# Kernel optimization log

Hardware: AMD Instinct MI355X
Metric: run time of the kernel (lower is better)

The kernel has to match this reference:

```python
import jax, jax.numpy as jnp
import numpy as np

SR = 44100.0  # sample_rate from init_kwargs


def _alpha(tau_ms):
    # Eq. (10): alpha = exp(-1 / (tau_s * fs)), tau clamped to [0.1, 1000] ms
    tau_s = jnp.clip(tau_ms, 0.1, 1000.0) / 1000.0
    return jnp.exp(-1.0 / (tau_s * SR))


def _env(x, alpha, attack):
    # Nonlinear envelope follower (Eqs. 9-10).
    # attack=True  -> smooth attack (when |x| rising), instant decay
    # attack=False -> smooth decay  (when |x| falling), instant attack
    xa = jnp.abs(x)
    xs = jnp.moveaxis(xa, -1, 0)  # [T, B, C]
    y0 = jnp.zeros(xa.shape[:-1], xa.dtype)  # [B, C]

    def step(y_prev, xn):
        cond = (xn > y_prev) if attack else (xn < y_prev)
        y_curr = jnp.where(cond, (1.0 - alpha) * xn + alpha * y_prev, xn)
        return y_curr, y_curr

    _, ys = jax.lax.scan(step, y0, xs)
    return jnp.moveaxis(ys, 0, -1)  # [B, C, T]


def _db_to_amp(db):
    return jnp.power(10.0, db / 20.0)


def reference(x, tauAtc, tauDtc, nu, dBregDelta):
    # Temporal Contrast Enhancement (Weger et al., ICAD 2019, Eqs. 12-14).
    # high_pass_filter is the identity in the source, so sh = x.
    alpha_d = _alpha(jnp.clip(tauDtc, 1.0, 100.0))
    alpha_a = _alpha(jnp.clip(tauAtc, 1.0, 100.0))
    et_d = _env(x, alpha_d, attack=False)      # envd(sh)
    et_a = _env(et_d, alpha_a, attack=True)    # enva(et_d)
    nu_amp = _db_to_amp(jnp.clip(nu, -60.0, 0.0))
    et = jnp.maximum(et_d - et_a - nu_amp, 0.0)
    et_env = _env(et, alpha_d, attack=False)   # envd(et)
    reg = _db_to_amp(jnp.clip(dBregDelta, -120.0, -60.0))
    modulation = et / (et_env + reg)
    return x * modulation


def setup_inputs() -> dict:
    key = jax.random.key(0)
    x = jax.random.normal(key, (8, 32, 88200), dtype=jnp.float32)  # [B, C, T]
    return {
        "x": x,
        "tauAtc": jnp.float32(3.0),
        "tauDtc": jnp.float32(7.0),
        "nu": jnp.float32(-40.0),
        "dBregDelta": jnp.float32(-96.0),
    }
```

## Files before the change

### kernel.cpp

```cpp
#include <hip/hip_runtime.h>
#include <cmath>


typedef float f32x4 __attribute__((ext_vector_type(4)));

static constexpr int   kT  = 88200;
static constexpr float kSR = 44100.0f;

static constexpr int FS_      = 24;
static constexpr int FNC_     = kT / FS_;
static constexpr int FPADS    = FS_ + 4;
static constexpr int FTH      = 512;
static constexpr int FNT      = (FNC_ + FTH - 1) / FTH;
static constexpr int FTAILC   = FNC_ - FTH * (FNT - 1);
static constexpr int FF4C     = FS_ / 4;
static constexpr int FTILE_F4 = FTH * FF4C;
static constexpr int FTAIL_F4 = FTAILC * FF4C;
static constexpr int FBUF_F   = FTH * FPADS;

struct EnvP { float ad, bd, aa, ba, nuamp, reg; };

__device__ __forceinline__ EnvP make_params(const float* tauA, const float* tauD,
                                            const float* nu, const float* dbreg) {
  EnvP p;
  float td = fminf(fmaxf(tauD[0], 1.0f), 100.0f);
  td = fminf(fmaxf(td, 0.1f), 1000.0f) * 0.001f;
  float ta = fminf(fmaxf(tauA[0], 1.0f), 100.0f);
  ta = fminf(fmaxf(ta, 0.1f), 1000.0f) * 0.001f;
  p.ad = expf(-1.0f / (td * kSR));
  p.aa = expf(-1.0f / (ta * kSR));
  p.bd = 1.0f - p.ad;
  p.ba = 1.0f - p.aa;
  p.nuamp = exp10f(fminf(fmaxf(nu[0],    -60.0f),   0.0f) * 0.05f);
  p.reg   = exp10f(fminf(fmaxf(dbreg[0], -120.0f), -60.0f) * 0.05f);
  return p;
}

template <int MODE>
__device__ __forceinline__ void sweep(const float* __restrict__ xs,
                                      float* __restrict__ os,
                                      const EnvP& p,
                                      float* __restrict__ buf0,
                                      float* __restrict__ buf1,
                                      float* __restrict__ Ac, float* __restrict__ Bc,
                                      const float* __restrict__ Ydl,
                                      const float* __restrict__ Yal,
                                      const float* __restrict__ Yel,
                                      int t) {
  f32x4 r0, r1, r2, r3, r4, r5;
  const f32x4* xg4 = reinterpret_cast<const f32x4*>(xs);

#define LD_TILE(TILE)                                                        \
  do {                                                                       \
    const int nf4_ = ((TILE) == FNT - 1) ? FTAIL_F4 : FTILE_F4;              \
    const f32x4* xg_ = xg4 + (size_t)(TILE) * FTILE_F4;                      \
    int i0_ = t;                                                             \
    r0 = xg_[i0_ < nf4_ ? i0_ : 0];  i0_ += FTH;                             \
    r1 = xg_[i0_ < nf4_ ? i0_ : 0];  i0_ += FTH;                             \
    r2 = xg_[i0_ < nf4_ ? i0_ : 0];  i0_ += FTH;                             \
    r3 = xg_[i0_ < nf4_ ? i0_ : 0];  i0_ += FTH;                             \
    r4 = xg_[i0_ < nf4_ ? i0_ : 0];  i0_ += FTH;                             \
    r5 = xg_[i0_ < nf4_ ? i0_ : 0];                                          \
  } while (0)

#define WR_TILE(BUF)                                                         \
  do {                                                                       \
    float* b_ = (BUF);                                                       \
    int i0_ = t, ch_, of_;                                                   \
    ch_ = i0_ / FF4C; of_ = (i0_ - ch_ * FF4C) * 4;                          \
    *reinterpret_cast<f32x4*>(&b_[ch_ * FPADS + of_]) = r0;  i0_ += FTH;     \
    ch_ = i0_ / FF4C; of_ = (i0_ - ch_ * FF4C) * 4;                          \
    *reinterpret_cast<f32x4*>(&b_[ch_ * FPADS + of_]) = r1;  i0_ += FTH;     \
    ch_ = i0_ / FF4C; of_ = (i0_ - ch_ * FF4C) * 4;                          \
    *reinterpret_cast<f32x4*>(&b_[ch_ * FPADS + of_]) = r2;  i0_ += FTH;     \
    ch_ = i0_ / FF4C; of_ = (i0_ - ch_ * FF4C) * 4;                          \
    *reinterpret_cast<f32x4*>(&b_[ch_ * FPADS + of_]) = r3;  i0_ += FTH;     \
    ch_ = i0_ / FF4C; of_ = (i0_ - ch_ * FF4C) * 4;                          \
    *reinterpret_cast<f32x4*>(&b_[ch_ * FPADS + of_]) = r4;  i0_ += FTH;     \
    ch_ = i0_ / FF4C; of_ = (i0_ - ch_ * FF4C) * 4;                          \
    *reinterpret_cast<f32x4*>(&b_[ch_ * FPADS + of_]) = r5;                  \
  } while (0)

  LD_TILE(0);
  WR_TILE(buf0);
  __syncthreads();
  int cur = 0;
  for (int it = 0; it < FNT; ++it) {
    const bool pf = (it + 1 < FNT);
    if (pf) LD_TILE(it + 1);
    __builtin_amdgcn_sched_barrier(0);
    float* bc = cur ? buf1 : buf0;
    float* bn = cur ? buf0 : buf1;
    const int c = it * FTH + t;
    if (c < FNC_) {
      float* my = &bc[t * FPADS];
      if (MODE == 0) {
        float A = -INFINITY, B = 0.0f;
#pragma unroll 2
        for (int i = 0; i < FF4C; ++i) {
          f32x4 v = *reinterpret_cast<const f32x4*>(&my[4 * i]);
#pragma unroll
          for (int j = 0; j < 4; ++j) {
            float xa = fabsf(v[j]);
            float bx = p.bd * xa;
            A = fmaxf(xa, fmaf(p.ad, A, bx));
            B = fmaf(p.ad, B, bx);
          }
        }
        Ac[c] = A; Bc[c] = B;
      } else if (MODE == 1) {
        float yd = Ydl[c];
        float A = INFINITY, B = 0.0f;
#pragma unroll 2
        for (int i = 0; i < FF4C; ++i) {
          f32x4 v = *reinterpret_cast<const f32x4*>(&my[4 * i]);
#pragma unroll
          for (int j = 0; j < 4; ++j) {
            float xa = fabsf(v[j]);
            yd = fmaxf(xa, fmaf(p.ad, yd, p.bd * xa));
            float by = p.ba * yd;
            A = fminf(yd, fmaf(p.aa, A, by));
            B = fmaf(p.aa, B, by);
          }
        }
        Ac[c] = A; Bc[c] = B;
      } else if (MODE == 2) {
        float yd = Ydl[c], ya = Yal[c];
        float A = -INFINITY, B = 0.0f;
#pragma unroll 2
        for (int i = 0; i < FF4C; ++i) {
          f32x4 v = *reinterpret_cast<const f32x4*>(&my[4 * i]);
#pragma unroll
          for (int j = 0; j < 4; ++j) {
            float xa = fabsf(v[j]);
            yd = fmaxf(xa, fmaf(p.ad, yd, p.bd * xa));
            ya = fminf(yd, fmaf(p.aa, ya, p.ba * yd));
            float et = fmaxf((yd - ya) - p.nuamp, 0.0f);
            float bx = p.bd * et;
            A = fmaxf(et, fmaf(p.ad, A, bx));
            B = fmaf(p.ad, B, bx);
          }
        }
        Ac[c] = A; Bc[c] = B;
      } else {
        float yd = Ydl[c], ya = Yal[c], ye = Yel[c];
#pragma unroll 2
        for (int i = 0; i < FF4C; ++i) {
          f32x4 v = *reinterpret_cast<const f32x4*>(&my[4 * i]);
          f32x4 oo;
#pragma unroll
          for (int j = 0; j < 4; ++j) {
            float xa = fabsf(v[j]);
            yd = fmaxf(xa, fmaf(p.ad, yd, p.bd * xa));
            ya = fminf(yd, fmaf(p.aa, ya, p.ba * yd));
            float et = fmaxf((yd - ya) - p.nuamp, 0.0f);
            ye = fmaxf(et, fmaf(p.ad, ye, p.bd * et));
            oo[j] = v[j] * (et / (ye + p.reg));
          }
          *reinterpret_cast<f32x4*>(&my[4 * i]) = oo;
        }
      }
    }
    if (MODE == 3) {
      __syncthreads();
      f32x4* og = reinterpret_cast<f32x4*>(os) + (size_t)it * FTILE_F4;
      const int nf4 = pf ? FTILE_F4 : FTAIL_F4;
#pragma unroll
      for (int i = 0; i < FF4C; ++i) {
        int idx = t + i * FTH;
        if (idx < nf4) {
          int chunk = idx / FF4C;
          int off   = (idx - chunk * FF4C) * 4;
          f32x4 v = *reinterpret_cast<const f32x4*>(&bc[chunk * FPADS + off]);
          __builtin_nontemporal_store(v, &og[idx]);
        }
      }
    }
    if (pf) WR_TILE(bn);
    __syncthreads();
    cur ^= 1;
  }
#undef LD_TILE
#undef WR_TILE
}

template <int ATTACK>
__device__ __forceinline__ void scan_lds(const float* __restrict__ Ac,
                                         const float* __restrict__ Bc,
                                         float* __restrict__ Y,
                                         const EnvP& p,
                                         float* __restrict__ sbuf, int t) {
  constexpr int CPT = (FNC_ + FTH - 1) / FTH;
  const float alpha = ATTACK ? p.aa : p.ad;
  const float ID_A  = ATTACK ? INFINITY : -INFINITY;
  const float gS = powf(alpha, (float)FS_);

  float ca[CPT], cb[CPT];
  float a = ID_A, b = 0.0f, g = 1.0f;
#pragma unroll
  for (int k = 0; k < CPT; ++k) {
    int c = t * CPT + k;
    if (c < FNC_) { ca[k] = Ac[c]; cb[k] = Bc[c]; }
    else          { ca[k] = ID_A;  cb[k] = 0.0f; }
    float cg = (c < FNC_) ? gS : 1.0f;
    float na = ATTACK ? fminf(ca[k], fmaf(cg, a, cb[k]))
                      : fmaxf(ca[k], fmaf(cg, a, cb[k]));
    b = fmaf(cg, b, cb[k]);
    g = cg * g;
    a = na;
  }

  float* sA = sbuf; float* sB = sbuf + FTH; float* sG = sbuf + 2 * FTH;
  sA[t] = a; sB[t] = b; sG[t] = g;
  __syncthreads();
#pragma unroll
  for (int d = 1; d < FTH; d <<= 1) {
    float pa = 0.0f, pb = 0.0f, pg = 0.0f;
    if (t >= d) { pa = sA[t - d]; pb = sB[t - d]; pg = sG[t - d]; }
    __syncthreads();
    if (t >= d) {
      float na = ATTACK ? fminf(a, fmaf(g, pa, b)) : fmaxf(a, fmaf(g, pa, b));
      b = fmaf(g, pb, b);
      g = g * pg;
      a = na;
      sA[t] = a; sB[t] = b; sG[t] = g;
    }
    __syncthreads();
  }

  float ea, eb;
  if (t == 0) { ea = ID_A; eb = 0.0f; }
  else        { ea = sA[t - 1]; eb = sB[t - 1]; }

#pragma unroll
  for (int k = 0; k < CPT; ++k) {
    int c = t * CPT + k;
    if (c >= FNC_) break;
    Y[c] = ATTACK ? fminf(ea, eb) : fmaxf(ea, eb);
    float na = ATTACK ? fminf(ca[k], fmaf(gS, ea, cb[k]))
                      : fmaxf(ca[k], fmaf(gS, ea, cb[k]));
    eb = fmaf(gS, eb, cb[k]);
    ea = na;
  }
}

__global__
__attribute__((amdgpu_flat_work_group_size(512, 512), amdgpu_waves_per_eu(2, 2)))
void k_one(const float* __restrict__ x,
           const float* tauA, const float* tauD,
           const float* nu, const float* dbreg,
           float* __restrict__ Ydg, float* __restrict__ Yag,
           float* __restrict__ Yeg,
           float* __restrict__ out) {
  extern __shared__ float lds[];
  float* buf0 = lds;
  float* buf1 = lds + FBUF_F;
  float* Ac   = lds + 2 * FBUF_F;
  float* Bc   = Ac + FNC_;
  const int t = threadIdx.x;
  const int s = blockIdx.x;
  const float* xs = x   + (size_t)s * kT;
  float*       os = out + (size_t)s * kT;
  float* Yd = Ydg + (size_t)s * FNC_;
  float* Ya = Yag + (size_t)s * FNC_;
  float* Ye = Yeg + (size_t)s * FNC_;
  EnvP p = make_params(tauA, tauD, nu, dbreg);

  sweep<0>(xs, nullptr, p, buf0, buf1, Ac, Bc, nullptr, nullptr, nullptr, t);
  scan_lds<0>(Ac, Bc, Yd, p, buf0, t);
  __syncthreads();
  sweep<1>(xs, nullptr, p, buf0, buf1, Ac, Bc, Yd, nullptr, nullptr, t);
  scan_lds<1>(Ac, Bc, Ya, p, buf0, t);
  __syncthreads();
  sweep<2>(xs, nullptr, p, buf0, buf1, Ac, Bc, Yd, Ya, nullptr, t);
  scan_lds<0>(Ac, Bc, Ye, p, buf0, t);
  __syncthreads();
  sweep<3>(xs, os, p, buf0, buf1, Ac, Bc, Yd, Ya, Ye, t);
}

template <int FS, int MODE>
__global__ __launch_bounds__(256)
void k_pass(const float* __restrict__ x,
            const float* tauA, const float* tauD,
            const float* nu, const float* dbreg,
            const float* __restrict__ FYd, const float* __restrict__ FYa,
            const float* __restrict__ FYe,
            float* __restrict__ O0, float* __restrict__ O1) {
  constexpr int FP = FS + 4;
  __shared__ float lds[256 * FP];
  const int t   = threadIdx.x;
  const int blk = blockIdx.x;
  const size_t tileBase = (size_t)blk * (256 * FS);
  const float4* xg = reinterpret_cast<const float4*>(x + tileBase);
#pragma unroll
  for (int i = 0; i < FS / 4; ++i) {
    int idx = t + i * 256;
    float4 v = xg[idx];
    int chunk = (idx * 4) / FS;
    int off   = idx * 4 - chunk * FS;
    *reinterpret_cast<float4*>(&lds[chunk * FP + off]) = v;
  }
  __syncthreads();
  EnvP p = make_params(tauA, tauD, nu, dbreg);
  const int gchunk = blk * 256 + t;
  float* my = &lds[t * FP];
  if (MODE == 0) {
    float A = -INFINITY, B = 0.0f;
#pragma unroll 2
    for (int i = 0; i < FS / 4; ++i) {
      float4 v = *reinterpret_cast<const float4*>(&my[4 * i]);
      float vv[4] = {v.x, v.y, v.z, v.w};
#pragma unroll
      for (int j = 0; j < 4; ++j) {
        float xa = fabsf(vv[j]);
        float bx = p.bd * xa;
        A = fmaxf(xa, fmaf(p.ad, A, bx));
        B = fmaf(p.ad, B, bx);
      }
    }
    O0[gchunk] = A; O1[gchunk] = B;
  } else if (MODE == 1) {
    float yd = FYd[gchunk];
    float A = INFINITY, B = 0.0f;
#pragma unroll 2
    for (int i = 0; i < FS / 4; ++i) {
      float4 v = *reinterpret_cast<const float4*>(&my[4 * i]);
      float vv[4] = {v.x, v.y, v.z, v.w};
#pragma unroll
      for (int j = 0; j < 4; ++j) {
        float xa = fabsf(vv[j]);
        yd = fmaxf(xa, fmaf(p.ad, yd, p.bd * xa));
        float by = p.ba * yd;
        A = fminf(yd, fmaf(p.aa, A, by));
        B = fmaf(p.aa, B, by);
      }
    }
    O0[gchunk] = A; O1[gchunk] = B;
  } else if (MODE == 2) {
    float yd = FYd[gchunk], ya = FYa[gchunk];
    float A = -INFINITY, B = 0.0f;
#pragma unroll 2
    for (int i = 0; i < FS / 4; ++i) {
      float4 v = *reinterpret_cast<const float4*>(&my[4 * i]);
      float vv[4] = {v.x, v.y, v.z, v.w};
#pragma unroll
      for (int j = 0; j < 4; ++j) {
        float xa = fabsf(vv[j]);
        yd = fmaxf(xa, fmaf(p.ad, yd, p.bd * xa));
        ya = fminf(yd, fmaf(p.aa, ya, p.ba * yd));
        float et = fmaxf((yd - ya) - p.nuamp, 0.0f);
        float bx = p.bd * et;
        A = fmaxf(et, fmaf(p.ad, A, bx));
        B = fmaf(p.ad, B, bx);
      }
    }
    O0[gchunk] = A; O1[gchunk] = B;
  } else {
    float yd = FYd[gchunk], ya = FYa[gchunk], ye = FYe[gchunk];
#pragma unroll 2
    for (int i = 0; i < FS / 4; ++i) {
      float4 v = *reinterpret_cast<const float4*>(&my[4 * i]);
      float vv[4] = {v.x, v.y, v.z, v.w};
      float oo[4];
#pragma unroll
      for (int j = 0; j < 4; ++j) {
        float xa = fabsf(vv[j]);
        yd = fmaxf(xa, fmaf(p.ad, yd, p.bd * xa));
        ya = fminf(yd, fmaf(p.aa, ya, p.ba * yd));
        float et = fmaxf((yd - ya) - p.nuamp, 0.0f);
        ye = fmaxf(et, fmaf(p.ad, ye, p.bd * et));
        oo[j] = vv[j] * (et / (ye + p.reg));
      }
      *reinterpret_cast<float4*>(&my[4 * i]) = make_float4(oo[0], oo[1], oo[2], oo[3]);
    }
    __syncthreads();
    float4* og = reinterpret_cast<float4*>(O0 + tileBase);
#pragma unroll
    for (int i = 0; i < FS / 4; ++i) {
      int idx = t + i * 256;
      int chunk = (idx * 4) / FS;
      int off   = idx * 4 - chunk * FS;
      og[idx] = *reinterpret_cast<const float4*>(&lds[chunk * FP + off]);
    }
  }
}

template <int FS, int ATTACK>
__global__ __launch_bounds__(256)
void k_scan(const float* __restrict__ A, const float* __restrict__ B,
            float* __restrict__ Y,
            const float* tauA, const float* tauD,
            const float* nu, const float* dbreg) {
  constexpr int FNC = kT / FS;
  constexpr int CPT = (FNC + 255) / 256;
  EnvP p = make_params(tauA, tauD, nu, dbreg);
  const float alpha = ATTACK ? p.aa : p.ad;
  const float ID_A  = ATTACK ? INFINITY : -INFINITY;
  int s = blockIdx.x, t = threadIdx.x;
  long base = (long)s * FNC;
  float gS = powf(alpha, (float)FS);

  float ca[CPT], cb[CPT];
  float a = ID_A, b = 0.0f, g = 1.0f;
#pragma unroll
  for (int k = 0; k < CPT; ++k) {
    int c = t * CPT + k;
    if (c < FNC) { ca[k] = A[base + c]; cb[k] = B[base + c]; }
    else         { ca[k] = ID_A;        cb[k] = 0.0f; }
    float cg = (c < FNC) ? gS : 1.0f;
    float na = ATTACK ? fminf(ca[k], fmaf(cg, a, cb[k]))
                      : fmaxf(ca[k], fmaf(cg, a, cb[k]));
    b = fmaf(cg, b, cb[k]);
    g = cg * g;
    a = na;
  }

  __shared__ float sA[256], sB[256], sG[256];
  sA[t] = a; sB[t] = b; sG[t] = g;
  __syncthreads();
#pragma unroll
  for (int d = 1; d < 256; d <<= 1) {
    float pa = 0.0f, pb = 0.0f, pg = 0.0f;
    if (t >= d) { pa = sA[t - d]; pb = sB[t - d]; pg = sG[t - d]; }
    __syncthreads();
    if (t >= d) {
      float na = ATTACK ? fminf(a, fmaf(g, pa, b)) : fmaxf(a, fmaf(g, pa, b));
      b = fmaf(g, pb, b);
      g = g * pg;
      a = na;
      sA[t] = a; sB[t] = b; sG[t] = g;
    }
    __syncthreads();
  }

  float ea, eb;
  if (t == 0) { ea = ID_A; eb = 0.0f; }
  else        { ea = sA[t - 1]; eb = sB[t - 1]; }

#pragma unroll
  for (int k = 0; k < CPT; ++k) {
    int c = t * CPT + k;
    if (c >= FNC) break;
    Y[base + c] = ATTACK ? fminf(ea, eb) : fmaxf(ea, eb);
    float na = ATTACK ? fminf(ca[k], fmaf(gS, ea, cb[k]))
                      : fmaxf(ca[k], fmaf(gS, ea, cb[k]));
    eb = fmaf(gS, eb, cb[k]);
    ea = na;
  }
}

template <int FS>
static void run_pipeline(const float* x, const float* tauA, const float* tauD,
                         const float* nu, const float* dbreg, float* out,
                         float* wsf, int nseries, hipStream_t stream) {
  const int nc  = kT / FS;
  const int nch = nseries * nc;
  float* A   = wsf;
  float* B   = wsf + (size_t)nch;
  float* FYd = wsf + (size_t)2 * nch;
  float* FYa = wsf + (size_t)3 * nch;
  float* FYe = wsf + (size_t)4 * nch;
  const int grid = nch / 256;

  k_pass<FS, 0><<<grid, 256, 0, stream>>>(x, tauA, tauD, nu, dbreg, nullptr, nullptr, nullptr, A, B);
  k_scan<FS, 0><<<nseries, 256, 0, stream>>>(A, B, FYd, tauA, tauD, nu, dbreg);
  k_pass<FS, 1><<<grid, 256, 0, stream>>>(x, tauA, tauD, nu, dbreg, FYd, nullptr, nullptr, A, B);
  k_scan<FS, 1><<<nseries, 256, 0, stream>>>(A, B, FYa, tauA, tauD, nu, dbreg);
  k_pass<FS, 2><<<grid, 256, 0, stream>>>(x, tauA, tauD, nu, dbreg, FYd, FYa, nullptr, A, B);
  k_scan<FS, 0><<<nseries, 256, 0, stream>>>(A, B, FYe, tauA, tauD, nu, dbreg);
  k_pass<FS, 3><<<grid, 256, 0, stream>>>(x, tauA, tauD, nu, dbreg, FYd, FYa, FYe, out, nullptr);
}

extern "C" void kernel_launch(void* const* d_in, const int* in_sizes, int n_in,
                              void* d_out, int out_size, void* d_ws, size_t ws_size,
                              hipStream_t stream) {
  const float* x     = (const float*)d_in[0];
  const float* tauA  = (const float*)d_in[1];
  const float* tauD  = (const float*)d_in[2];
  const float* nu    = (const float*)d_in[3];
  const float* dbreg = (const float*)d_in[4];
  float* out = (float*)d_out;
  float* wsf = (float*)d_ws;
  const int nseries = in_sizes[0] / kT;

  constexpr size_t LDSZ = (size_t)(2 * FBUF_F + 2 * FNC_) * sizeof(float);
  const size_t NS = (size_t)FNC_ * nseries;
  const bool wsOK = 3 * NS * sizeof(float) <= ws_size;

  static int fusedOK = -1;
  if (fusedOK < 0) {
    hipFuncSetAttribute(reinterpret_cast<const void*>(&k_one),
                        hipFuncAttributeMaxDynamicSharedMemorySize, (int)LDSZ);
    (void)hipGetLastError();
    fusedOK = 1;
  }

  if (fusedOK == 1 && wsOK) {
    float* Yd = wsf;
    float* Ya = wsf + NS;
    float* Ye = wsf + 2 * NS;
    k_one<<<nseries, FTH, LDSZ, stream>>>(x, tauA, tauD, nu, dbreg, Yd, Ya, Ye, out);
    if (hipGetLastError() == hipSuccess) return;
    fusedOK = 0;
  }

  auto fits = [&](int FS) {
    return (size_t)5 * nseries * (kT / FS) * sizeof(float) <= ws_size;
  };
  if      (fits(40))  run_pipeline<40 >(x, tauA, tauD, nu, dbreg, out, wsf, nseries, stream);
  else if (fits(56))  run_pipeline<56 >(x, tauA, tauD, nu, dbreg, out, wsf, nseries, stream);
  else if (fits(72))  run_pipeline<72 >(x, tauA, tauD, nu, dbreg, out, wsf, nseries, stream);
  else                run_pipeline<120>(x, tauA, tauD, nu, dbreg, out, wsf, nseries, stream);
}
```

Before: 226.8 us.

## Replace LDS double-buffered tile staging with direct per-thread global loads

The fused per-series kernel no longer stages input tiles through double-buffered LDS with a register prefetch. Each thread now loads its 24-sample chunk directly from global memory as six float4 loads, and in the final pass writes output straight to global with nontemporal stores. Block size doubles to 1024 threads with static LDS, and the dynamic-LDS attribute setup and fallback check are dropped. This removes LDS traffic and most barriers, but each thread's loads are strided across lanes, so coalescing is worse and latency hiding now depends on occupancy instead of explicit prefetch.

Result: slower. 400.2 us (+76.4%).

```diff
diff --git a/kernel.cpp b/kernel.cpp
--- a/kernel.cpp
+++ b/kernel.cpp
@@ -7,16 +7,11 @@
 static constexpr int   kT  = 88200;
 static constexpr float kSR = 44100.0f;
 
-static constexpr int FS_      = 24;
-static constexpr int FNC_     = kT / FS_;
-static constexpr int FPADS    = FS_ + 4;
-static constexpr int FTH      = 512;
-static constexpr int FNT      = (FNC_ + FTH - 1) / FTH;
-static constexpr int FTAILC   = FNC_ - FTH * (FNT - 1);
-static constexpr int FF4C     = FS_ / 4;
-static constexpr int FTILE_F4 = FTH * FF4C;
-static constexpr int FTAIL_F4 = FTAILC * FF4C;
-static constexpr int FBUF_F   = FTH * FPADS;
+static constexpr int FS_    = 24;
+static constexpr int FNC_   = kT / FS_;
+static constexpr int FTH    = 1024;
+static constexpr int FNT    = (FNC_ + FTH - 1) / FTH;
+static constexpr int FF4C   = FS_ / 4;
 
 struct EnvP { float ad, bd, aa, ba, nuamp, reg; };
 
@@ -40,148 +35,87 @@
 __device__ __forceinline__ void sweep(const float* __restrict__ xs,
                                       float* __restrict__ os,
                                       const EnvP& p,
-                                      float* __restrict__ buf0,
-                                      float* __restrict__ buf1,
                                       float* __restrict__ Ac, float* __restrict__ Bc,
                                       const float* __restrict__ Ydl,
                                       const float* __restrict__ Yal,
                                       const float* __restrict__ Yel,
                                       int t) {
-  f32x4 r0, r1, r2, r3, r4, r5;
   const f32x4* xg4 = reinterpret_cast<const f32x4*>(xs);
-
-#define LD_TILE(TILE)                                                        \
-  do {                                                                       \
-    const int nf4_ = ((TILE) == FNT - 1) ? FTAIL_F4 : FTILE_F4;              \
-    const f32x4* xg_ = xg4 + (size_t)(TILE) * FTILE_F4;                      \
-    int i0_ = t;                                                             \
-    r0 = xg_[i0_ < nf4_ ? i0_ : 0];  i0_ += FTH;                             \
-    r1 = xg_[i0_ < nf4_ ? i0_ : 0];  i0_ += FTH;                             \
-    r2 = xg_[i0_ < nf4_ ? i0_ : 0];  i0_ += FTH;                             \
-    r3 = xg_[i0_ < nf4_ ? i0_ : 0];  i0_ += FTH;                             \
-    r4 = xg_[i0_ < nf4_ ? i0_ : 0];  i0_ += FTH;                             \
-    r5 = xg_[i0_ < nf4_ ? i0_ : 0];                                          \
-  } while (0)
-
-#define WR_TILE(BUF)                                                         \
-  do {                                                                       \
-    float* b_ = (BUF);                                                       \
-    int i0_ = t, ch_, of_;                                                   \
-    ch_ = i0_ / FF4C; of_ = (i0_ - ch_ * FF4C) * 4;                          \
-    *reinterpret_cast<f32x4*>(&b_[ch_ * FPADS + of_]) = r0;  i0_ += FTH;     \
-    ch_ = i0_ / FF4C; of_ = (i0_ - ch_ * FF4C) * 4;                          \
-    *reinterpret_cast<f32x4*>(&b_[ch_ * FPADS + of_]) = r1;  i0_ += FTH;     \
-    ch_ = i0_ / FF4C; of_ = (i0_ - ch_ * FF4C) * 4;                          \
-    *reinterpret_cast<f32x4*>(&b_[ch_ * FPADS + of_]) = r2;  i0_ += FTH;     \
-    ch_ = i0_ / FF4C; of_ = (i0_ - ch_ * FF4C) * 4;                          \
-    *reinterpret_cast<f32x4*>(&b_[ch_ * FPADS + of_]) = r3;  i0_ += FTH;     \
-    ch_ = i0_ / FF4C; of_ = (i0_ - ch_ * FF4C) * 4;                          \
-    *reinterpret_cast<f32x4*>(&b_[ch_ * FPADS + of_]) = r4;  i0_ += FTH;     \
-    ch_ = i0_ / FF4C; of_ = (i0_ - ch_ * FF4C) * 4;                          \
-    *reinterpret_cast<f32x4*>(&b_[ch_ * FPADS + of_]) = r5;                  \
-  } while (0)
-
-  LD_TILE(0);
-  WR_TILE(buf0);
-  __syncthreads();
-  int cur = 0;
+#pragma unroll
   for (int it = 0; it < FNT; ++it) {
-    const bool pf = (it + 1 < FNT);
-    if (pf) LD_TILE(it + 1);
-    __builtin_amdgcn_sched_barrier(0);
-    float* bc = cur ? buf1 : buf0;
-    float* bn = cur ? buf0 : buf1;
     const int c = it * FTH + t;
     if (c < FNC_) {
-      float* my = &bc[t * FPADS];
+      const f32x4* xc = xg4 + (size_t)c * FF4C;
+      f32x4 v0 = xc[0], v1 = xc[1], v2 = xc[2],
+            v3 = xc[3], v4 = xc[4], v5 = xc[5];
       if (MODE == 0) {
         float A = -INFINITY, B = 0.0f;
-#pragma unroll 2
-        for (int i = 0; i < FF4C; ++i) {
-          f32x4 v = *reinterpret_cast<const f32x4*>(&my[4 * i]);
-#pragma unroll
-          for (int j = 0; j < 4; ++j) {
-            float xa = fabsf(v[j]);
-            float bx = p.bd * xa;
-            A = fmaxf(xa, fmaf(p.ad, A, bx));
-            B = fmaf(p.ad, B, bx);
-          }
-        }
+#define STEP0(V)                                                             \
+  _Pragma("unroll")                                                          \
+  for (int j = 0; j < 4; ++j) {                                              \
+    float xa = fabsf((V)[j]);                                                \
+    float bx = p.bd * xa;                                                    \
+    A = fmaxf(xa, fmaf(p.ad, A, bx));                                        \
+    B = fmaf(p.ad, B, bx);                                                   \
+  }
+        STEP0(v0) STEP0(v1) STEP0(v2) STEP0(v3) STEP0(v4) STEP0(v5)
+#undef STEP0
         Ac[c] = A; Bc[c] = B;
       } else if (MODE == 1) {
         float yd = Ydl[c];
         float A = INFINITY, B = 0.0f;
-#pragma unroll 2
-        for (int i = 0; i < FF4C; ++i) {
-          f32x4 v = *reinterpret_cast<const f32x4*>(&my[4 * i]);
-#pragma unroll
-          for (int j = 0; j < 4; ++j) {
-            float xa = fabsf(v[j]);
-            yd = fmaxf(xa, fmaf(p.ad, yd, p.bd * xa));
-            float by = p.ba * yd;
-            A = fminf(yd, fmaf(p.aa, A, by));
-            B = fmaf(p.aa, B, by);
-          }
-        }
+#define STEP1(V)                                                             \
+  _Pragma("unroll")                                                          \
+  for (int j = 0; j < 4; ++j) {                                              \
+    float xa = fabsf((V)[j]);                                                \
+    yd = fmaxf(xa, fmaf(p.ad, yd, p.bd * xa));                               \
+    float by = p.ba * yd;                                                    \
+    A = fminf(yd, fmaf(p.aa, A, by));                                        \
+    B = fmaf(p.aa, B, by);                                                   \
+  }
+        STEP1(v0) STEP1(v1) STEP1(v2) STEP1(v3) STEP1(v4) STEP1(v5)
+#undef STEP1
         Ac[c] = A; Bc[c] = B;
       } else if (MODE == 2) {
         float yd = Ydl[c], ya = Yal[c];
         float A = -INFINITY, B = 0.0f;
-#pragma unroll 2
-        for (int i = 0; i < FF4C; ++i) {
-          f32x4 v = *reinterpret_cast<const f32x4*>(&my[4 * i]);
-#pragma unroll
-          for (int j = 0; j < 4; ++j) {
-            float xa = fabsf(v[j]);
-            yd = fmaxf(xa, fmaf(p.ad, yd, p.bd * xa));
-            ya = fminf(yd, fmaf(p.aa, ya, p.ba * yd));
-            float et = fmaxf((yd - ya) - p.nuamp, 0.0f);
-            float bx = p.bd * et;
-            A = fmaxf(et, fmaf(p.ad, A, bx));
-            B = fmaf(p.ad, B, bx);
-          }
-        }
+#define STEP2(V)                                                             \
+  _Pragma("unroll")                                                          \
+  for (int j = 0; j < 4; ++j) {                                              \
+    float xa = fabsf((V)[j]);                                                \
+    yd = fmaxf(xa, fmaf(p.ad, yd, p.bd * xa));                               \
+    ya = fminf(yd, fmaf(p.aa, ya, p.ba * yd));                               \
+    float et = fmaxf((yd - ya) - p.nuamp, 0.0f);                             \
+    float bx = p.bd * et;                                                    \
+    A = fmaxf(et, fmaf(p.ad, A, bx));                                        \
+    B = fmaf(p.ad, B, bx);                                                   \
+  }
+        STEP2(v0) STEP2(v1) STEP2(v2) STEP2(v3) STEP2(v4) STEP2(v5)
+#undef STEP2
         Ac[c] = A; Bc[c] = B;
       } else {
         float yd = Ydl[c], ya = Yal[c], ye = Yel[c];
-#pragma unroll 2
-        for (int i = 0; i < FF4C; ++i) {
-          f32x4 v = *reinterpret_cast<const f32x4*>(&my[4 * i]);
-          f32x4 oo;
-#pragma unroll
-          for (int j = 0; j < 4; ++j) {
-            float xa = fabsf(v[j]);
-            yd = fmaxf(xa, fmaf(p.ad, yd, p.bd * xa));
-            ya = fminf(yd, fmaf(p.aa, ya, p.ba * yd));
-            float et = fmaxf((yd - ya) - p.nuamp, 0.0f);
-            ye = fmaxf(et, fmaf(p.ad, ye, p.bd * et));
-            oo[j] = v[j] * (et / (ye + p.reg));
-          }
-          *reinterpret_cast<f32x4*>(&my[4 * i]) = oo;
-        }
+        f32x4* oc = reinterpret_cast<f32x4*>(os) + (size_t)c * FF4C;
+#define STEP3(V, OIDX)                                                       \
+  {                                                                          \
+    f32x4 oo;                                                                \
+    _Pragma("unroll")                                                        \
+    for (int j = 0; j < 4; ++j) {                                            \
+      float xa = fabsf((V)[j]);                                              \
+      yd = fmaxf(xa, fmaf(p.ad, yd, p.bd * xa));                             \
+      ya = fminf(yd, fmaf(p.aa, ya, p.ba * yd));                             \
+      float et = fmaxf((yd - ya) - p.nuamp, 0.0f);                           \
+      ye = fmaxf(et, fmaf(p.ad, ye, p.bd * et));                             \
+      oo[j] = (V)[j] * (et / (ye + p.reg));                                  \
+    }                                                                        \
+    __builtin_nontemporal_store(oo, &oc[OIDX]);                              \
+  }
+        STEP3(v0, 0) STEP3(v1, 1) STEP3(v2, 2)
+        STEP3(v3, 3) STEP3(v4, 4) STEP3(v5, 5)
+#undef STEP3
       }
     }
-    if (MODE == 3) {
-      __syncthreads();
-      f32x4* og = reinterpret_cast<f32x4*>(os) + (size_t)it * FTILE_F4;
-      const int nf4 = pf ? FTILE_F4 : FTAIL_F4;
-#pragma unroll
-      for (int i = 0; i < FF4C; ++i) {
-        int idx = t + i * FTH;
-        if (idx < nf4) {
-          int chunk = idx / FF4C;
-          int off   = (idx - chunk * FF4C) * 4;
-          f32x4 v = *reinterpret_cast<const f32x4*>(&bc[chunk * FPADS + off]);
-          __builtin_nontemporal_store(v, &og[idx]);
-        }
-      }
-    }
-    if (pf) WR_TILE(bn);
-    __syncthreads();
-    cur ^= 1;
-  }
-#undef LD_TILE
-#undef WR_TILE
+  }
 }
 
 template <int ATTACK>
@@ -245,18 +179,16 @@
 }
 
 __global__
-__attribute__((amdgpu_flat_work_group_size(512, 512), amdgpu_waves_per_eu(2, 2)))
+__attribute__((amdgpu_flat_work_group_size(1024, 1024), amdgpu_waves_per_eu(4, 4)))
 void k_one(const float* __restrict__ x,
            const float* tauA, const float* tauD,
            const float* nu, const float* dbreg,
            float* __restrict__ Ydg, float* __restrict__ Yag,
            float* __restrict__ Yeg,
            float* __restrict__ out) {
-  extern __shared__ float lds[];
-  float* buf0 = lds;
-  float* buf1 = lds + FBUF_F;
-  float* Ac   = lds + 2 * FBUF_F;
-  float* Bc   = Ac + FNC_;
+  __shared__ float Ac[FNC_];
+  __shared__ float Bc[FNC_];
+  __shared__ float sbuf[3 * FTH];
   const int t = threadIdx.x;
   const int s = blockIdx.x;
   const float* xs = x   + (size_t)s * kT;
@@ -266,16 +198,19 @@
   float* Ye = Yeg + (size_t)s * FNC_;
   EnvP p = make_params(tauA, tauD, nu, dbreg);
 
-  sweep<0>(xs, nullptr, p, buf0, buf1, Ac, Bc, nullptr, nullptr, nullptr, t);
-  scan_lds<0>(Ac, Bc, Yd, p, buf0, t);
-  __syncthreads();
-  sweep<1>(xs, nullptr, p, buf0, buf1, Ac, Bc, Yd, nullptr, nullptr, t);
-  scan_lds<1>(Ac, Bc, Ya, p, buf0, t);
-  __syncthreads();
-  sweep<2>(xs, nullptr, p, buf0, buf1, Ac, Bc, Yd, Ya, nullptr, t);
-  scan_lds<0>(Ac, Bc, Ye, p, buf0, t);
-  __syncthreads();
-  sweep<3>(xs, os, p, buf0, buf1, Ac, Bc, Yd, Ya, Ye, t);
+  sweep<0>(xs, nullptr, p, Ac, Bc, nullptr, nullptr, nullptr, t);
+  __syncthreads();
+  scan_lds<0>(Ac, Bc, Yd, p, sbuf, t);
+  __syncthreads();
+  sweep<1>(xs, nullptr, p, Ac, Bc, Yd, nullptr, nullptr, t);
+  __syncthreads();
+  scan_lds<1>(Ac, Bc, Ya, p, sbuf, t);
+  __syncthreads();
+  sweep<2>(xs, nullptr, p, Ac, Bc, Yd, Ya, nullptr, t);
+  __syncthreads();
+  scan_lds<0>(Ac, Bc, Ye, p, sbuf, t);
+  __syncthreads();
+  sweep<3>(xs, os, p, Ac, Bc, Yd, Ya, Ye, t);
 }
 
 template <int FS, int MODE>
@@ -483,25 +418,15 @@
   float* wsf = (float*)d_ws;
   const int nseries = in_sizes[0] / kT;
 
-  constexpr size_t LDSZ = (size_t)(2 * FBUF_F + 2 * FNC_) * sizeof(float);
   const size_t NS = (size_t)FNC_ * nseries;
   const bool wsOK = 3 * NS * sizeof(float) <= ws_size;
 
-  static int fusedOK = -1;
-  if (fusedOK < 0) {
-    hipFuncSetAttribute(reinterpret_cast<const void*>(&k_one),
-                        hipFuncAttributeMaxDynamicSharedMemorySize, (int)LDSZ);
-    (void)hipGetLastError();
-    fusedOK = 1;
-  }
-
-  if (fusedOK == 1 && wsOK) {
+  if (wsOK) {
     float* Yd = wsf;
     float* Ya = wsf + NS;
     float* Ye = wsf + 2 * NS;
-    k_one<<<nseries, FTH, LDSZ, stream>>>(x, tauA, tauD, nu, dbreg, Yd, Ya, Ye, out);
-    if (hipGetLastError() == hipSuccess) return;
-    fusedOK = 0;
+    k_one<<<nseries, FTH, 0, stream>>>(x, tauA, tauD, nu, dbreg, Yd, Ya, Ye, out);
+    return;
   }
 
   auto fits = [&](int FS) {
```
